# Kernel tuning notes

Measured on AMD Instinct MI355X. Metric: run time of the kernel, lower is better.

Reference implementation:

```python
import jax, jax.numpy as jnp
import numpy as np

ACT_DIM = 768
DICT_SIZE = 16384
K = 64
BATCH = 2048


def setup_inputs() -> dict:
    key = jax.random.key(0)
    k_x, k_w, k_be = jax.random.split(key, 3)
    x = jax.random.normal(k_x, (BATCH, ACT_DIM), dtype=jnp.float32)
    # encoder weight [dict_size, act_dim]; decoder initialized as encoder.T with unit-norm columns
    W_enc = jax.random.normal(k_w, (DICT_SIZE, ACT_DIM), dtype=jnp.float32) * 0.02
    b_enc = jnp.zeros((DICT_SIZE,), dtype=jnp.float32)
    W_dec = W_enc.T  # [act_dim, dict_size]
    eps = jnp.finfo(jnp.float32).eps
    W_dec = W_dec / (jnp.linalg.norm(W_dec, axis=0, keepdims=True) + eps)
    b_dec = jnp.zeros((ACT_DIM,), dtype=jnp.float32)
    return {"x": x, "W_enc": W_enc, "b_enc": b_enc, "W_dec": W_dec, "b_dec": b_dec}


def reference(x, W_enc, b_enc, W_dec, b_dec):
    B = x.shape[0]
    # encode: linear on (x - b_dec), relu
    post_relu_BF = jax.nn.relu((x - b_dec) @ W_enc.T + b_enc)  # [B, F]
    flat = post_relu_BF.reshape(-1)  # [B*F]
    # global batch top-k: keep k*B largest activations across the whole batch
    vals, idx = jax.lax.top_k(flat, K * B)
    encoded_flat = jnp.zeros_like(flat).at[idx].set(vals)
    encoded_BF = encoded_flat.reshape(post_relu_BF.shape)
    # decode
    x_hat_BD = encoded_BF @ W_dec.T + b_dec  # [B, D]
    return x_hat_BD
```

## Files before the change

### kernel.cpp

```cpp
#include <hip/hip_runtime.h>
#include <stdint.h>

#define BATCH   2048
#define DIM     768
#define FEAT    16384
#define KSEL    64
#define KB_SEL  (BATCH * KSEL)
#define N_TOT   (BATCH * FEAT)
#define NX4     (BATCH * DIM / 4)
#define NW4     (FEAT * DIM / 4)

#define GBM 128
#define GBN 128
#define GBK 32
#define AROW   24
#define APLANE 3088

#define SAMP_N  3072
#define CCAP    262144
#define TIE_CAP 1024
#define LSTAGE  2048
#define FG      8
#define FBLK    (CCAP / (FG * 4))

#define SL_T32    0
#define SL_NC     1
#define SL_DEF    2
#define SL_NTIE   3
#define SL_WIN    4
#define SL_S0     16

typedef __attribute__((ext_vector_type(8))) __bf16 bf16x8;
typedef __attribute__((ext_vector_type(4))) float  f32x4;
typedef unsigned long long u64;

__device__ __forceinline__ unsigned short bf16r(float v)
{
    unsigned u = __float_as_uint(v);
    u += 0x7FFFu + ((u >> 16) & 1u);
    return (unsigned short)(u >> 16);
}

__device__ __forceinline__ unsigned wave_append(unsigned* counter, bool pred)
{
    unsigned long long m = __ballot(pred);
    if (m == 0ull) return 0xFFFFFFFFu;
    const int lane = threadIdx.x & 63;
    const int leader = __ffsll((unsigned long long)m) - 1;
    unsigned base = 0;
    if (lane == leader) base = atomicAdd(counter, (unsigned)__popcll(m));
    base = __shfl(base, leader, 64);
    if (!pred) return 0xFFFFFFFFu;
    return base + (unsigned)__popcll(m & ((1ull << lane) - 1ull));
}

__global__ __launch_bounds__(256) void sae17_prep(const float* __restrict__ x,
                                                  const float* __restrict__ Wenc,
                                                  const float* __restrict__ bdec,
                                                  unsigned short* __restrict__ xb,
                                                  unsigned short* __restrict__ wb)
{
    const int tot = NX4 + NW4;
    for (int i = blockIdx.x * 256 + threadIdx.x; i < tot; i += gridDim.x * 256) {
        if (i < NX4) {
            const int e = i * 4;
            const int d = e % DIM;
            float4 v  = *(const float4*)(x + e);
            float4 dv = *(const float4*)(bdec + d);
            uint2 p;
            p.x = (unsigned)bf16r(v.x - dv.x) | ((unsigned)bf16r(v.y - dv.y) << 16);
            p.y = (unsigned)bf16r(v.z - dv.z) | ((unsigned)bf16r(v.w - dv.w) << 16);
            *(uint2*)(xb + e) = p;
        } else {
            const int e = (i - NX4) * 4;
            float4 v = *(const float4*)(Wenc + e);
            uint2 p;
            p.x = (unsigned)bf16r(v.x) | ((unsigned)bf16r(v.y) << 16);
            p.y = (unsigned)bf16r(v.z) | ((unsigned)bf16r(v.w) << 16);
            *(uint2*)(wb + e) = p;
        }
    }
}

__global__ __launch_bounds__(256) void sae17_gemm(const unsigned short* __restrict__ xb,
                                                  const unsigned short* __restrict__ wb,
                                                  const float* __restrict__ benc,
                                                  unsigned short* __restrict__ Yb)
{
    __shared__ unsigned short Als[4 * APLANE];
    __shared__ unsigned short Bls[4 * APLANE];

    const int tid  = threadIdx.x;
    const int row0 = blockIdx.y * GBM;
    const int col0 = blockIdx.x * GBN;
    const int wid  = tid >> 6;
    const int lane = tid & 63;
    const int wr = wid >> 1;
    const int wc = wid & 1;
    const int fr = lane & 15;
    const int kg = lane >> 4;

    f32x4 acc[4][4];
#pragma unroll
    for (int i = 0; i < 4; ++i)
#pragma unroll
        for (int j = 0; j < 4; ++j) acc[i][j] = (f32x4){0.f, 0.f, 0.f, 0.f};

    for (int kt = 0; kt < DIM; kt += GBK) {
#pragma unroll
        for (int i = 0; i < 4; ++i) {
            const int idx = i * 256 + tid;
            const int r   = idx >> 3;
            const int kq  = (idx & 7) * 4;
            const int g   = kq >> 3;
            const int k0  = kq & 7;
            *(uint2*)&Als[g * APLANE + r * AROW + k0] =
                *(const uint2*)(xb + (size_t)(row0 + r) * DIM + kt + kq);
            *(uint2*)&Bls[g * APLANE + r * AROW + k0] =
                *(const uint2*)(wb + (size_t)(col0 + r) * DIM + kt + kq);
        }
        __syncthreads();

        bf16x8 afr[4], bfr[4];
#pragma unroll
        for (int mi = 0; mi < 4; ++mi)
            afr[mi] = *(const bf16x8*)&Als[kg * APLANE + (wr * 64 + mi * 16 + fr) * AROW];
#pragma unroll
        for (int ni = 0; ni < 4; ++ni)
            bfr[ni] = *(const bf16x8*)&Bls[kg * APLANE + (wc * 64 + ni * 16 + fr) * AROW];
#pragma unroll
        for (int mi = 0; mi < 4; ++mi)
#pragma unroll
            for (int ni = 0; ni < 4; ++ni)
                acc[mi][ni] = __builtin_amdgcn_mfma_f32_16x16x32_bf16(
                    afr[mi], bfr[ni], acc[mi][ni], 0, 0, 0);
        __syncthreads();
    }

#pragma unroll
    for (int ni = 0; ni < 4; ++ni) {
        const int col = col0 + wc * 64 + ni * 16 + fr;
        const float be = benc[col];
#pragma unroll
        for (int mi = 0; mi < 4; ++mi) {
            const int rbase = row0 + wr * 64 + mi * 16 + kg * 4;
#pragma unroll
            for (int j = 0; j < 4; ++j)
                Yb[(size_t)(rbase + j) * FEAT + col] =
                    bf16r(fmaxf(acc[mi][ni][j] + be, 0.f));
        }
    }
}

__global__ void sae17_wt(const float* __restrict__ Wdec,
                         unsigned short* __restrict__ Wtb)
{
    __shared__ float t[32][33];
    const int f0 = blockIdx.x * 32;
    const int d0 = blockIdx.y * 32;
    const int tx = threadIdx.x;
    const int ty = threadIdx.y;
#pragma unroll
    for (int i = 0; i < 4; ++i)
        t[ty + i * 8][tx] = Wdec[(size_t)(d0 + ty + i * 8) * FEAT + f0 + tx];
    __syncthreads();
#pragma unroll
    for (int i = 0; i < 4; ++i)
        Wtb[(size_t)(f0 + ty + i * 8) * DIM + d0 + tx] = bf16r(t[tx][ty + i * 8]);
}

__global__ __launch_bounds__(256) void sae17_shist(const unsigned short* __restrict__ Yb,
                                                   unsigned* __restrict__ hist)
{
    __shared__ unsigned h[8192];
    const int t = threadIdx.x;
    for (int i = t; i < 8192; i += 256) h[i] = 0u;
    __syncthreads();
    const uint4* Y8 = (const uint4*)Yb;
    const int idx = blockIdx.x * 256 + t;
    const int i = idx * 64;
    if (i < N_TOT / 8) {
        uint4 v = Y8[i];
        unsigned w[4] = {v.x, v.y, v.z, v.w};
#pragma unroll
        for (int k = 0; k < 4; ++k) {
            unsigned lo = w[k] & 0xFFFFu;
            unsigned hi = w[k] >> 16;
            if (lo) atomicAdd(&h[lo >> 2], 1u);
            if (hi) atomicAdd(&h[hi >> 2], 1u);
        }
    }
    __syncthreads();
    for (int i2 = t; i2 < 8192; i2 += 256) {
        unsigned c = h[i2];
        if (c) atomicAdd(&hist[i2], c);
    }
}

__global__ __launch_bounds__(1024) void sae17_selb(const unsigned* __restrict__ hist,
                                                   unsigned* sl)
{
    __shared__ unsigned s[1024];
    const int t = threadIdx.x;
    const int C = 8;
    const unsigned N = (unsigned)SAMP_N;
    const int lo = t * C;
    unsigned S = 0;
    for (int i = 0; i < C; ++i) S += hist[lo + i];
    s[t] = S;
    __syncthreads();
    for (int off = 1; off < 1024; off <<= 1) {
        unsigned v = (t + off < 1024) ? s[t + off] : 0u;
        __syncthreads();
        s[t] += v;
        __syncthreads();
    }
    const unsigned incl  = s[t];
    const unsigned above = incl - S;
    if (above < N && N <= incl) {
        unsigned cum = above;
        for (int i = lo + C - 1; i >= lo; --i) {
            cum += hist[i];
            if (cum >= N) { sl[SL_T32] = (unsigned)i << 2; break; }
        }
    }
}

__global__ __launch_bounds__(256) void sae17_cand(const unsigned short* __restrict__ Yb,
                                                  unsigned* __restrict__ sl,
                                                  int* __restrict__ cand_raw)
{
    __shared__ int      loc[LSTAGE];
    __shared__ unsigned lcnt;
    __shared__ unsigned gbase;
    if (threadIdx.x == 0) lcnt = 0;
    __syncthreads();

    const unsigned T = sl[SL_T32];
    const uint4* Y8 = (const uint4*)Yb;
    const int total8 = N_TOT / 8;
    for (int i = blockIdx.x * blockDim.x + threadIdx.x; i < total8;
         i += gridDim.x * blockDim.x) {
        uint4 v = Y8[i];
        unsigned w[4] = {v.x, v.y, v.z, v.w};
#pragma unroll
        for (int k = 0; k < 4; ++k) {
            unsigned lo = w[k] & 0xFFFFu;
            unsigned hi = w[k] >> 16;
            if (lo >= T) {
                unsigned p = atomicAdd(&lcnt, 1u);
                if (p < (unsigned)LSTAGE) loc[p] = i * 8 + k * 2;
            }
            if (hi >= T) {
                unsigned p = atomicAdd(&lcnt, 1u);
                if (p < (unsigned)LSTAGE) loc[p] = i * 8 + k * 2 + 1;
            }
        }
    }
    __syncthreads();
    unsigned n = lcnt;
    if (n > (unsigned)LSTAGE) n = (unsigned)LSTAGE;
    if (threadIdx.x == 0) gbase = atomicAdd(&sl[SL_NC], n);
    __syncthreads();
    const unsigned base = gbase;
    for (unsigned k = threadIdx.x; k < n; k += blockDim.x) {
        unsigned dst = base + k;
        if (dst < (unsigned)CCAP) cand_raw[dst] = loc[k];
    }
}

__global__ __launch_bounds__(256) void sae17_fhist(const int* __restrict__ cand_raw,
                                                   const unsigned* __restrict__ sl,
                                                   unsigned* __restrict__ fhist)
{
    __shared__ unsigned h[16384];
    const int t = threadIdx.x;
    for (int i = t; i < 16384; i += 256) h[i] = 0u;
    __syncthreads();
    unsigned NC = sl[SL_NC];
    if (NC > (unsigned)CCAP) NC = (unsigned)CCAP;
    for (int i = blockIdx.x * 256 + t; i < (int)NC; i += gridDim.x * 256)
        atomicAdd(&h[cand_raw[i] & (FEAT - 1)], 1u);
    __syncthreads();
    for (int i = t; i < 16384; i += 256) {
        unsigned c = h[i];
        if (c) atomicAdd(&fhist[i], c);
    }
}

__global__ __launch_bounds__(1024) void sae17_fscan(const unsigned* __restrict__ fhist,
                                                    unsigned* __restrict__ fofs)
{
    __shared__ unsigned s[1024];
    const int t = threadIdx.x;
    unsigned c[16];
    unsigned sum = 0;
#pragma unroll
    for (int j = 0; j < 16; ++j) { c[j] = fhist[t * 16 + j]; sum += c[j]; }
    s[t] = sum;
    __syncthreads();
    for (int off = 1; off < 1024; off <<= 1) {
        unsigned v = (t >= off) ? s[t - off] : 0u;
        __syncthreads();
        s[t] += v;
        __syncthreads();
    }
    unsigned run = s[t] - sum;
#pragma unroll
    for (int j = 0; j < 16; ++j) { fofs[t * 16 + j] = run; run += c[j]; }
}

__global__ __launch_bounds__(256) void sae17_fscat(const int* __restrict__ cand_raw,
                                                   const unsigned* __restrict__ sl,
                                                   const unsigned* __restrict__ fofs,
                                                   unsigned* __restrict__ fcur,
                                                   int* __restrict__ cand_flat)
{
    unsigned NC = sl[SL_NC];
    if (NC > (unsigned)CCAP) NC = (unsigned)CCAP;
    for (int i = blockIdx.x * 256 + threadIdx.x; i < (int)NC; i += gridDim.x * 256) {
        int flat = cand_raw[i];
        int f = flat & (FEAT - 1);
        unsigned p = atomicAdd(&fcur[f], 1u);
        unsigned dst = fofs[f] + p;
        if (dst < (unsigned)CCAP) cand_flat[dst] = flat;
    }
}

__global__ __launch_bounds__(256) void sae17_feval(const float* __restrict__ x,
                                                   const float* __restrict__ Wenc,
                                                   const float* __restrict__ benc,
                                                   const float* __restrict__ bdec,
                                                   const unsigned* __restrict__ sl,
                                                   const int* __restrict__ cand_flat,
                                                   u64* __restrict__ cand_key)
{
    unsigned NC = sl[SL_NC];
    if (NC > (unsigned)CCAP) NC = (unsigned)CCAP;
    const int lane = threadIdx.x & 63;
    const int b = blockIdx.x;
    const int lb = (b & 7) * (FBLK / 8) + (b >> 3);
    const int wid = lb * 4 + (threadIdx.x >> 6);
    const int c0 = wid * FG;
    if (c0 >= (int)NC) return;

    float bd[12], wv[12];
#pragma unroll
    for (int j = 0; j < 12; ++j) bd[j] = bdec[lane + j * 64];
    int fprev = -1;

    for (int g = 0; g < FG; ++g) {
        const int c = c0 + g;
        if (c >= (int)NC) break;
        const int flat = cand_flat[c];
        const int bb = flat >> 14;
        const int f  = flat & (FEAT - 1);
        if (f != fprev) {
            const float* wr = Wenc + (size_t)f * DIM;
#pragma unroll
            for (int j = 0; j < 12; ++j) wv[j] = wr[lane + j * 64];
            fprev = f;
        }
        const float* xr = x + (size_t)bb * DIM;
        double p = 0.0;
#pragma unroll
        for (int j = 0; j < 12; ++j)
            p = fma((double)xr[lane + j * 64] - (double)bd[j], (double)wv[j], p);
#pragma unroll
        for (int o = 32; o > 0; o >>= 1) p += __shfl_xor(p, o, 64);
        if (lane == 0) {
            p += (double)benc[f];
            if (p < 0.0) p = 0.0;
            cand_key[c] = (u64)__double_as_longlong(p);
        }
    }
}

__global__ __launch_bounds__(256) void sae17_hist64(const u64* __restrict__ cand_key,
                                                    const unsigned* __restrict__ sl,
                                                    unsigned* __restrict__ hist,
                                                    int pass)
{
    __shared__ unsigned h[16384];
    const int t = threadIdx.x;
    for (int i = t; i < 16384; i += 256) h[i] = 0u;
    __syncthreads();

    unsigned NC = sl[SL_NC];
    if (NC > (unsigned)CCAP) NC = (unsigned)CCAP;
    u64 pref = 0;
    for (int i = 0; i < pass; ++i) pref = (pref << 14) | (u64)sl[SL_S0 + i];
    const int chk_sh = 64 - 14 * pass;
    const int bkt_sh = 50 - 14 * pass;

    for (int i = blockIdx.x * 256 + t; i < (int)NC; i += gridDim.x * 256) {
        u64 key = cand_key[i];
        if (pass > 0 && (key >> chk_sh) != pref) continue;
        atomicAdd(&h[(unsigned)(key >> bkt_sh) & 0x3FFFu], 1u);
    }
    __syncthreads();
    for (int i = t; i < 16384; i += 256) {
        unsigned c = h[i];
        if (c) atomicAdd(&hist[i], c);
    }
}

__global__ __launch_bounds__(1024) void sae17_sel14(const unsigned* __restrict__ hist,
                                                    unsigned* sl, int pass)
{
    __shared__ unsigned s[1024];
    const int t = threadIdx.x;
    const int C = 16;
    const unsigned N = (pass == 0) ? (unsigned)KB_SEL : sl[SL_S0 + 4 + pass - 1];
    const int lo = t * C;
    unsigned S = 0;
    for (int i = 0; i < C; ++i) S += hist[lo + i];
    s[t] = S;
    __syncthreads();
    for (int off = 1; off < 1024; off <<= 1) {
        unsigned v = (t + off < 1024) ? s[t + off] : 0u;
        __syncthreads();
        s[t] += v;
        __syncthreads();
    }
    const unsigned incl  = s[t];
    const unsigned above = incl - S;
    if (above < N && N <= incl) {
        unsigned cum = above;
        for (int i = lo + C - 1; i >= lo; --i) {
            cum += hist[i];
            if (cum >= N) {
                sl[SL_S0 + pass]     = (unsigned)i;
                sl[SL_S0 + 4 + pass] = N - (cum - hist[i]);
                break;
            }
        }
    }
}

__global__ __launch_bounds__(256) void sae17_maxb(const u64* __restrict__ cand_key,
                                                  const unsigned* __restrict__ sl,
                                                  u64* __restrict__ mx)
{
    unsigned NC = sl[SL_NC];
    if (NC > (unsigned)CCAP) NC = (unsigned)CCAP;
    const u64 Tsh1 = ((u64)sl[SL_S0 + 0] << 28) | ((u64)sl[SL_S0 + 1] << 14) |
                     (u64)sl[SL_S0 + 2];
    u64 m = 0;
    for (int i = blockIdx.x * 256 + threadIdx.x; i < (int)NC; i += gridDim.x * 256) {
        u64 k = cand_key[i];
        if ((k >> 22) < Tsh1 && k > m) m = k;
    }
#pragma unroll
    for (int o = 32; o > 0; o >>= 1) {
        u64 o2 = __shfl_xor(m, o, 64);
        if (o2 > m) m = o2;
    }
    if ((threadIdx.x & 63) == 0 && m) atomicMax((unsigned long long*)mx, m);
}

__global__ __launch_bounds__(256) void sae17_class(const u64* __restrict__ cand_key,
                                                   const int* __restrict__ cand_flat,
                                                   const u64* __restrict__ mx,
                                                   unsigned* __restrict__ sl,
                                                   unsigned* __restrict__ row_cnt,
                                                   int* __restrict__ sel_flat,
                                                   float* __restrict__ sel_val,
                                                   int* __restrict__ tie_flat,
                                                   u64* __restrict__ tie_key)
{
    unsigned NC = sl[SL_NC];
    if (NC > (unsigned)CCAP) NC = (unsigned)CCAP;
    const u64 Tsh1 = ((u64)sl[SL_S0 + 0] << 28) | ((u64)sl[SL_S0 + 1] << 14) |
                     (u64)sl[SL_S0 + 2];
    const u64 Tsh2 = mx[0] >> 22;
    const int c = blockIdx.x * 256 + threadIdx.x;
    const bool active = (c < (int)NC);
    u64 key = 0;
    int flat = 0;
    u64 keysh = 0;
    if (active) {
        key = cand_key[c];
        keysh = key >> 22;
        flat = cand_flat[c];
    }
    const bool selp = active && (keysh > Tsh1);
    unsigned p = wave_append(&sl[SL_DEF], selp);
    if (selp && p < (unsigned)KB_SEL) {
        sel_flat[p] = flat;
        sel_val[p]  = (float)__longlong_as_double((long long)key);
        atomicAdd(&row_cnt[flat >> 14], 1u);
    }
    const bool tiep = active && !selp && (keysh == Tsh2);
    unsigned q = wave_append(&sl[SL_NTIE], tiep);
    if (tiep && q < (unsigned)TIE_CAP) { tie_flat[q] = flat; tie_key[q] = key; }
}

__global__ __launch_bounds__(256) void sae17_ties(const int* __restrict__ tie_flat,
                                                  const u64* __restrict__ tie_key,
                                                  unsigned* __restrict__ sl,
                                                  int* __restrict__ sel_flat,
                                                  float* __restrict__ sel_val,
                                                  unsigned* __restrict__ row_cnt)
{
    unsigned R = sl[SL_NTIE];
    if (R > (unsigned)TIE_CAP) R = (unsigned)TIE_CAP;
    const unsigned REM = sl[SL_S0 + 6];
    const unsigned D = sl[SL_DEF];
    const int c = blockIdx.x * blockDim.x + threadIdx.x;
    if (c >= (int)R) return;
    const int ic = tie_flat[c];
    unsigned rank = 0;
    for (int j = 0; j < (int)R; ++j)
        if (tie_flat[j] < ic) ++rank;
    if (rank < REM) {
        unsigned p = D + atomicAdd(&sl[SL_WIN], 1u);
        if (p < (unsigned)KB_SEL) {
            sel_flat[p] = ic;
            sel_val[p]  = (float)__longlong_as_double((long long)tie_key[c]);
            atomicAdd(&row_cnt[ic >> 14], 1u);
        }
    }
}

__global__ __launch_bounds__(256) void sae17_scan(const unsigned* __restrict__ row_cnt,
                                                  unsigned* __restrict__ row_ofs)
{
    __shared__ unsigned s[256];
    const int t = threadIdx.x;
    unsigned c[8];
    unsigned sum = 0;
#pragma unroll
    for (int j = 0; j < 8; ++j) { c[j] = row_cnt[t * 8 + j]; sum += c[j]; }
    s[t] = sum;
    __syncthreads();
    for (int off = 1; off < 256; off <<= 1) {
        unsigned v = (t >= off) ? s[t - off] : 0u;
        __syncthreads();
        s[t] += v;
        __syncthreads();
    }
    unsigned run = s[t] - sum;
#pragma unroll
    for (int j = 0; j < 8; ++j) { row_ofs[t * 8 + j] = run; run += c[j]; }
    if (t == 255) row_ofs[2048] = run;
}

__global__ void sae17_scatter(const int* __restrict__ sel_flat,
                              const float* __restrict__ sel_val,
                              const unsigned* __restrict__ row_ofs,
                              unsigned* __restrict__ cursor,
                              int* __restrict__ gf, float* __restrict__ gv)
{
    int e = blockIdx.x * blockDim.x + threadIdx.x;
    if (e >= KB_SEL) return;
    int flat = sel_flat[e];
    int b = flat >> 14;
    unsigned p = atomicAdd(&cursor[b], 1u);
    unsigned dst = row_ofs[b] + p;
    if (dst < (unsigned)KB_SEL) {
        gf[dst] = flat & (FEAT - 1);
        gv[dst] = sel_val[e];
    }
}

__global__ __launch_bounds__(256) void sae17_decode(const int* __restrict__ gf,
                                                    const float* __restrict__ gv,
                                                    const unsigned* __restrict__ row_ofs,
                                                    const unsigned short* __restrict__ Wtb,
                                                    const float* __restrict__ bdec,
                                                    float* __restrict__ out)
{
    const int b = blockIdx.x;
    const int t = threadIdx.x;
    float a0 = 0.f, a1 = 0.f, a2 = 0.f;
    const unsigned s = row_ofs[b];
    const unsigned e = row_ofs[b + 1];
    for (unsigned i = s; i < e; ++i) {
        const int f   = gf[i];
        const float v = gv[i];
        const unsigned short* w = Wtb + (size_t)f * DIM;
        a0 = fmaf(v, __uint_as_float((unsigned)w[t]       << 16), a0);
        a1 = fmaf(v, __uint_as_float((unsigned)w[t + 256] << 16), a1);
        a2 = fmaf(v, __uint_as_float((unsigned)w[t + 512] << 16), a2);
    }
    out[(size_t)b * DIM + t]       = a0 + bdec[t];
    out[(size_t)b * DIM + t + 256] = a1 + bdec[t + 256];
    out[(size_t)b * DIM + t + 512] = a2 + bdec[t + 512];
}

extern "C" void kernel_launch(void* const* d_in, const int* in_sizes, int n_in,
                              void* d_out, int out_size, void* d_ws, size_t ws_size,
                              hipStream_t stream)
{
    (void)in_sizes; (void)n_in; (void)out_size;
    const float* x    = (const float*)d_in[0];
    const float* Wenc = (const float*)d_in[1];
    const float* benc = (const float*)d_in[2];
    const float* Wdec = (const float*)d_in[3];
    const float* bdec = (const float*)d_in[4];
    float* out = (float*)d_out;

    char* ws = (char*)d_ws;
    size_t off = 0;
    unsigned short* Yb  = (unsigned short*)(ws + off);     off += (size_t)N_TOT * 2;
    unsigned short* Wtb = (unsigned short*)(ws + off);     off += (size_t)FEAT * DIM * 2;
    unsigned short* xb  = (unsigned short*)(ws + off);     off += (size_t)BATCH * DIM * 2;
    unsigned short* wb  = (unsigned short*)(ws + off);     off += (size_t)FEAT * DIM * 2;
    u64*      cand_key  = (u64*)(ws + off);                off += (size_t)CCAP * 8;
    int*      cand_raw  = (int*)(ws + off);                off += (size_t)CCAP * 4;
    int*      cand_flat = (int*)(ws + off);                off += (size_t)CCAP * 4;
    int*      tie_flat  = (int*)(ws + off);                off += (size_t)TIE_CAP * 4;
    u64*      tie_key   = (u64*)(ws + off);                off += (size_t)TIE_CAP * 8;
    unsigned* row_ofs   = (unsigned*)(ws + off);           off += 2052 * 4;
    unsigned* fofs      = (unsigned*)(ws + off);           off += 16384 * 4;
    char* zstart = ws + off;
    int*      sel_flat  = (int*)(ws + off);                off += (size_t)KB_SEL * 4;
    float*    sel_val   = (float*)(ws + off);              off += (size_t)KB_SEL * 4;
    int*      gf        = (int*)(ws + off);                off += (size_t)KB_SEL * 4;
    float*    gv        = (float*)(ws + off);              off += (size_t)KB_SEL * 4;
    unsigned* hist1     = (unsigned*)(ws + off);           off += 8192 * 4;
    unsigned* h64       = (unsigned*)(ws + off);           off += 3 * 16384 * 4;
    unsigned* fhist     = (unsigned*)(ws + off);           off += 16384 * 4;
    unsigned* fcur      = (unsigned*)(ws + off);           off += 16384 * 4;
    unsigned* row_cnt   = (unsigned*)(ws + off);           off += 2048 * 4;
    unsigned* cursor    = (unsigned*)(ws + off);           off += 2048 * 4;
    u64*      mx        = (u64*)(ws + off);                off += 8;
    unsigned* sl        = (unsigned*)(ws + off);           off += 256;
    const size_t zbytes = (size_t)((ws + off) - zstart);
    if (ws_size < off) return;

    hipMemsetAsync(zstart, 0, zbytes, stream);

    sae17_prep<<<4096, 256, 0, stream>>>(x, Wenc, bdec, xb, wb);
    sae17_wt<<<dim3(FEAT / 32, DIM / 32), dim3(32, 8), 0, stream>>>(Wdec, Wtb);
    sae17_gemm<<<dim3(FEAT / GBN, BATCH / GBM), 256, 0, stream>>>(xb, wb, benc, Yb);

    sae17_shist<<<256, 256, 0, stream>>>(Yb, hist1);
    sae17_selb<<<1, 1024, 0, stream>>>(hist1, sl);

    sae17_cand<<<2048, 256, 0, stream>>>(Yb, sl, cand_raw);
    sae17_fhist<<<256, 256, 0, stream>>>(cand_raw, sl, fhist);
    sae17_fscan<<<1, 1024, 0, stream>>>(fhist, fofs);
    sae17_fscat<<<256, 256, 0, stream>>>(cand_raw, sl, fofs, fcur, cand_flat);
    sae17_feval<<<FBLK, 256, 0, stream>>>(x, Wenc, benc, bdec, sl, cand_flat, cand_key);

    for (int p = 0; p < 3; ++p) {
        sae17_hist64<<<256, 256, 0, stream>>>(cand_key, sl, h64 + p * 16384, p);
        sae17_sel14<<<1, 1024, 0, stream>>>(h64 + p * 16384, sl, p);
    }
    sae17_maxb<<<256, 256, 0, stream>>>(cand_key, sl, mx);

    sae17_class<<<(CCAP + 255) / 256, 256, 0, stream>>>(cand_key, cand_flat, mx, sl, row_cnt,
                                                        sel_flat, sel_val, tie_flat, tie_key);
    sae17_ties<<<TIE_CAP / 256, 256, 0, stream>>>(tie_flat, tie_key, sl,
                                                  sel_flat, sel_val, row_cnt);

    sae17_scan<<<1, 256, 0, stream>>>(row_cnt, row_ofs);
    sae17_scatter<<<(KB_SEL + 255) / 256, 256, 0, stream>>>(sel_flat, sel_val, row_ofs, cursor, gf, gv);
    sae17_decode<<<BATCH, 256, 0, stream>>>(gf, gv, row_ofs, Wtb, bdec, out);
}
```

Measured before the change: 449.1 us.

## Fuse candidate thresholding into encoder GEMM and sample histogram from first row block

The full bf16 pre-activation matrix is no longer written to global memory. A first GEMM pass computes only the first 128 batch rows and builds the threshold histogram directly from its accumulators. A second full GEMM then applies the threshold in its epilogue and appends candidate indices, replacing the separate histogram and candidate scan kernels. This removes a large write and re-read of the activation matrix at the cost of extra GEMM work for the sample rows. It also makes the threshold estimate depend on the first rows being representative of the whole batch.

Result: faster. 434.7 us (-3.2%).

```diff
diff --git a/kernel.cpp b/kernel.cpp
--- a/kernel.cpp
+++ b/kernel.cpp
@@ -16,12 +16,13 @@
 #define AROW   24
 #define APLANE 3088
 
-#define SAMP_N  3072
-#define CCAP    262144
-#define TIE_CAP 1024
-#define LSTAGE  2048
-#define FG      8
-#define FBLK    (CCAP / (FG * 4))
+#define SAMP_ROWS 128
+#define SAMP_N    12288
+#define CCAP      262144
+#define TIE_CAP   1024
+#define LSTAGE    2048
+#define FG        8
+#define FBLK      (CCAP / (FG * 4))
 
 #define SL_T32    0
 #define SL_NC     1
@@ -54,7 +55,7 @@
     return base + (unsigned)__popcll(m & ((1ull << lane) - 1ull));
 }
 
-__global__ __launch_bounds__(256) void sae17_prep(const float* __restrict__ x,
+__global__ __launch_bounds__(256) void sae18_prep(const float* __restrict__ x,
                                                   const float* __restrict__ Wenc,
                                                   const float* __restrict__ bdec,
                                                   unsigned short* __restrict__ xb,
@@ -82,16 +83,18 @@
     }
 }
 
-__global__ __launch_bounds__(256) void sae17_gemm(const unsigned short* __restrict__ xb,
-                                                  const unsigned short* __restrict__ wb,
-                                                  const float* __restrict__ benc,
-                                                  unsigned short* __restrict__ Yb)
+__global__ __launch_bounds__(256) void sae18_sgemm(const unsigned short* __restrict__ xb,
+                                                   const unsigned short* __restrict__ wb,
+                                                   const float* __restrict__ benc,
+                                                   unsigned* __restrict__ hist)
 {
     __shared__ unsigned short Als[4 * APLANE];
     __shared__ unsigned short Bls[4 * APLANE];
+    __shared__ unsigned h[8192];
 
     const int tid  = threadIdx.x;
-    const int row0 = blockIdx.y * GBM;
+    for (int i = tid; i < 8192; i += 256) h[i] = 0u;
+    const int row0 = 0;
     const int col0 = blockIdx.x * GBN;
     const int wid  = tid >> 6;
     const int lane = tid & 63;
@@ -143,61 +146,21 @@
         const float be = benc[col];
 #pragma unroll
         for (int mi = 0; mi < 4; ++mi) {
-            const int rbase = row0 + wr * 64 + mi * 16 + kg * 4;
-#pragma unroll
-            for (int j = 0; j < 4; ++j)
-                Yb[(size_t)(rbase + j) * FEAT + col] =
-                    bf16r(fmaxf(acc[mi][ni][j] + be, 0.f));
-        }
-    }
-}
-
-__global__ void sae17_wt(const float* __restrict__ Wdec,
-                         unsigned short* __restrict__ Wtb)
-{
-    __shared__ float t[32][33];
-    const int f0 = blockIdx.x * 32;
-    const int d0 = blockIdx.y * 32;
-    const int tx = threadIdx.x;
-    const int ty = threadIdx.y;
-#pragma unroll
-    for (int i = 0; i < 4; ++i)
-        t[ty + i * 8][tx] = Wdec[(size_t)(d0 + ty + i * 8) * FEAT + f0 + tx];
-    __syncthreads();
-#pragma unroll
-    for (int i = 0; i < 4; ++i)
-        Wtb[(size_t)(f0 + ty + i * 8) * DIM + d0 + tx] = bf16r(t[tx][ty + i * 8]);
-}
-
-__global__ __launch_bounds__(256) void sae17_shist(const unsigned short* __restrict__ Yb,
-                                                   unsigned* __restrict__ hist)
-{
-    __shared__ unsigned h[8192];
-    const int t = threadIdx.x;
-    for (int i = t; i < 8192; i += 256) h[i] = 0u;
-    __syncthreads();
-    const uint4* Y8 = (const uint4*)Yb;
-    const int idx = blockIdx.x * 256 + t;
-    const int i = idx * 64;
-    if (i < N_TOT / 8) {
-        uint4 v = Y8[i];
-        unsigned w[4] = {v.x, v.y, v.z, v.w};
-#pragma unroll
-        for (int k = 0; k < 4; ++k) {
-            unsigned lo = w[k] & 0xFFFFu;
-            unsigned hi = w[k] >> 16;
-            if (lo) atomicAdd(&h[lo >> 2], 1u);
-            if (hi) atomicAdd(&h[hi >> 2], 1u);
-        }
-    }
-    __syncthreads();
-    for (int i2 = t; i2 < 8192; i2 += 256) {
-        unsigned c = h[i2];
-        if (c) atomicAdd(&hist[i2], c);
-    }
-}
-
-__global__ __launch_bounds__(1024) void sae17_selb(const unsigned* __restrict__ hist,
+#pragma unroll
+            for (int j = 0; j < 4; ++j) {
+                unsigned short bits = bf16r(fmaxf(acc[mi][ni][j] + be, 0.f));
+                if (bits) atomicAdd(&h[bits >> 2], 1u);
+            }
+        }
+    }
+    __syncthreads();
+    for (int i = tid; i < 8192; i += 256) {
+        unsigned c = h[i];
+        if (c) atomicAdd(&hist[i], c);
+    }
+}
+
+__global__ __launch_bounds__(1024) void sae18_selb(const unsigned* __restrict__ hist,
                                                    unsigned* sl)
 {
     __shared__ unsigned s[1024];
@@ -226,50 +189,114 @@
     }
 }
 
-__global__ __launch_bounds__(256) void sae17_cand(const unsigned short* __restrict__ Yb,
+__global__ __launch_bounds__(256) void sae18_gemm(const unsigned short* __restrict__ xb,
+                                                  const unsigned short* __restrict__ wb,
+                                                  const float* __restrict__ benc,
                                                   unsigned* __restrict__ sl,
                                                   int* __restrict__ cand_raw)
 {
+    __shared__ unsigned short Als[4 * APLANE];
+    __shared__ unsigned short Bls[4 * APLANE];
     __shared__ int      loc[LSTAGE];
     __shared__ unsigned lcnt;
     __shared__ unsigned gbase;
-    if (threadIdx.x == 0) lcnt = 0;
-    __syncthreads();
+
+    const int tid  = threadIdx.x;
+    if (tid == 0) lcnt = 0;
+    const int row0 = blockIdx.y * GBM;
+    const int col0 = blockIdx.x * GBN;
+    const int wid  = tid >> 6;
+    const int lane = tid & 63;
+    const int wr = wid >> 1;
+    const int wc = wid & 1;
+    const int fr = lane & 15;
+    const int kg = lane >> 4;
+
+    f32x4 acc[4][4];
+#pragma unroll
+    for (int i = 0; i < 4; ++i)
+#pragma unroll
+        for (int j = 0; j < 4; ++j) acc[i][j] = (f32x4){0.f, 0.f, 0.f, 0.f};
+
+    for (int kt = 0; kt < DIM; kt += GBK) {
+#pragma unroll
+        for (int i = 0; i < 4; ++i) {
+            const int idx = i * 256 + tid;
+            const int r   = idx >> 3;
+            const int kq  = (idx & 7) * 4;
+            const int g   = kq >> 3;
+            const int k0  = kq & 7;
+            *(uint2*)&Als[g * APLANE + r * AROW + k0] =
+                *(const uint2*)(xb + (size_t)(row0 + r) * DIM + kt + kq);
+            *(uint2*)&Bls[g * APLANE + r * AROW + k0] =
+                *(const uint2*)(wb + (size_t)(col0 + r) * DIM + kt + kq);
+        }
+        __syncthreads();
+
+        bf16x8 afr[4], bfr[4];
+#pragma unroll
+        for (int mi = 0; mi < 4; ++mi)
+            afr[mi] = *(const bf16x8*)&Als[kg * APLANE + (wr * 64 + mi * 16 + fr) * AROW];
+#pragma unroll
+        for (int ni = 0; ni < 4; ++ni)
+            bfr[ni] = *(const bf16x8*)&Bls[kg * APLANE + (wc * 64 + ni * 16 + fr) * AROW];
+#pragma unroll
+        for (int mi = 0; mi < 4; ++mi)
+#pragma unroll
+            for (int ni = 0; ni < 4; ++ni)
+                acc[mi][ni] = __builtin_amdgcn_mfma_f32_16x16x32_bf16(
+                    afr[mi], bfr[ni], acc[mi][ni], 0, 0, 0);
+        __syncthreads();
+    }
 
     const unsigned T = sl[SL_T32];
-    const uint4* Y8 = (const uint4*)Yb;
-    const int total8 = N_TOT / 8;
-    for (int i = blockIdx.x * blockDim.x + threadIdx.x; i < total8;
-         i += gridDim.x * blockDim.x) {
-        uint4 v = Y8[i];
-        unsigned w[4] = {v.x, v.y, v.z, v.w};
-#pragma unroll
-        for (int k = 0; k < 4; ++k) {
-            unsigned lo = w[k] & 0xFFFFu;
-            unsigned hi = w[k] >> 16;
-            if (lo >= T) {
-                unsigned p = atomicAdd(&lcnt, 1u);
-                if (p < (unsigned)LSTAGE) loc[p] = i * 8 + k * 2;
-            }
-            if (hi >= T) {
-                unsigned p = atomicAdd(&lcnt, 1u);
-                if (p < (unsigned)LSTAGE) loc[p] = i * 8 + k * 2 + 1;
+#pragma unroll
+    for (int ni = 0; ni < 4; ++ni) {
+        const int col = col0 + wc * 64 + ni * 16 + fr;
+        const float be = benc[col];
+#pragma unroll
+        for (int mi = 0; mi < 4; ++mi) {
+            const int rbase = row0 + wr * 64 + mi * 16 + kg * 4;
+#pragma unroll
+            for (int j = 0; j < 4; ++j) {
+                unsigned short bits = bf16r(fmaxf(acc[mi][ni][j] + be, 0.f));
+                if ((unsigned)bits >= T) {
+                    unsigned p = atomicAdd(&lcnt, 1u);
+                    if (p < (unsigned)LSTAGE) loc[p] = (rbase + j) * FEAT + col;
+                }
             }
         }
     }
     __syncthreads();
     unsigned n = lcnt;
     if (n > (unsigned)LSTAGE) n = (unsigned)LSTAGE;
-    if (threadIdx.x == 0) gbase = atomicAdd(&sl[SL_NC], n);
+    if (tid == 0) gbase = atomicAdd(&sl[SL_NC], n);
     __syncthreads();
     const unsigned base = gbase;
-    for (unsigned k = threadIdx.x; k < n; k += blockDim.x) {
+    for (unsigned k = tid; k < n; k += 256) {
         unsigned dst = base + k;
         if (dst < (unsigned)CCAP) cand_raw[dst] = loc[k];
     }
 }
 
-__global__ __launch_bounds__(256) void sae17_fhist(const int* __restrict__ cand_raw,
+__global__ void sae18_wt(const float* __restrict__ Wdec,
+                         unsigned short* __restrict__ Wtb)
+{
+    __shared__ float t[32][33];
+    const int f0 = blockIdx.x * 32;
+    const int d0 = blockIdx.y * 32;
+    const int tx = threadIdx.x;
+    const int ty = threadIdx.y;
+#pragma unroll
+    for (int i = 0; i < 4; ++i)
+        t[ty + i * 8][tx] = Wdec[(size_t)(d0 + ty + i * 8) * FEAT + f0 + tx];
+    __syncthreads();
+#pragma unroll
+    for (int i = 0; i < 4; ++i)
+        Wtb[(size_t)(f0 + ty + i * 8) * DIM + d0 + tx] = bf16r(t[tx][ty + i * 8]);
+}
+
+__global__ __launch_bounds__(256) void sae18_fhist(const int* __restrict__ cand_raw,
                                                    const unsigned* __restrict__ sl,
                                                    unsigned* __restrict__ fhist)
 {
@@ -288,7 +315,7 @@
     }
 }
 
-__global__ __launch_bounds__(1024) void sae17_fscan(const unsigned* __restrict__ fhist,
+__global__ __launch_bounds__(1024) void sae18_fscan(const unsigned* __restrict__ fhist,
                                                     unsigned* __restrict__ fofs)
 {
     __shared__ unsigned s[1024];
@@ -310,7 +337,7 @@
     for (int j = 0; j < 16; ++j) { fofs[t * 16 + j] = run; run += c[j]; }
 }
 
-__global__ __launch_bounds__(256) void sae17_fscat(const int* __restrict__ cand_raw,
+__global__ __launch_bounds__(256) void sae18_fscat(const int* __restrict__ cand_raw,
                                                    const unsigned* __restrict__ sl,
                                                    const unsigned* __restrict__ fofs,
                                                    unsigned* __restrict__ fcur,
@@ -327,7 +354,7 @@
     }
 }
 
-__global__ __launch_bounds__(256) void sae17_feval(const float* __restrict__ x,
+__global__ __launch_bounds__(256) void sae18_feval(const float* __restrict__ x,
                                                    const float* __restrict__ Wenc,
                                                    const float* __restrict__ benc,
                                                    const float* __restrict__ bdec,
@@ -376,7 +403,7 @@
     }
 }
 
-__global__ __launch_bounds__(256) void sae17_hist64(const u64* __restrict__ cand_key,
+__global__ __launch_bounds__(256) void sae18_hist64(const u64* __restrict__ cand_key,
                                                     const unsigned* __restrict__ sl,
                                                     unsigned* __restrict__ hist,
                                                     int pass)
@@ -405,7 +432,7 @@
     }
 }
 
-__global__ __launch_bounds__(1024) void sae17_sel14(const unsigned* __restrict__ hist,
+__global__ __launch_bounds__(1024) void sae18_sel14(const unsigned* __restrict__ hist,
                                                     unsigned* sl, int pass)
 {
     __shared__ unsigned s[1024];
@@ -438,7 +465,7 @@
     }
 }
 
-__global__ __launch_bounds__(256) void sae17_maxb(const u64* __restrict__ cand_key,
+__global__ __launch_bounds__(256) void sae18_maxb(const u64* __restrict__ cand_key,
                                                   const unsigned* __restrict__ sl,
                                                   u64* __restrict__ mx)
 {
@@ -459,7 +486,7 @@
     if ((threadIdx.x & 63) == 0 && m) atomicMax((unsigned long long*)mx, m);
 }
 
-__global__ __launch_bounds__(256) void sae17_class(const u64* __restrict__ cand_key,
+__global__ __launch_bounds__(256) void sae18_class(const u64* __restrict__ cand_key,
                                                    const int* __restrict__ cand_flat,
                                                    const u64* __restrict__ mx,
                                                    unsigned* __restrict__ sl,
@@ -496,7 +523,7 @@
     if (tiep && q < (unsigned)TIE_CAP) { tie_flat[q] = flat; tie_key[q] = key; }
 }
 
-__global__ __launch_bounds__(256) void sae17_ties(const int* __restrict__ tie_flat,
+__global__ __launch_bounds__(256) void sae18_ties(const int* __restrict__ tie_flat,
                                                   const u64* __restrict__ tie_key,
                                                   unsigned* __restrict__ sl,
                                                   int* __restrict__ sel_flat,
@@ -523,7 +550,7 @@
     }
 }
 
-__global__ __launch_bounds__(256) void sae17_scan(const unsigned* __restrict__ row_cnt,
+__global__ __launch_bounds__(256) void sae18_scan(const unsigned* __restrict__ row_cnt,
                                                   unsigned* __restrict__ row_ofs)
 {
     __shared__ unsigned s[256];
@@ -546,7 +573,7 @@
     if (t == 255) row_ofs[2048] = run;
 }
 
-__global__ void sae17_scatter(const int* __restrict__ sel_flat,
+__global__ void sae18_scatter(const int* __restrict__ sel_flat,
                               const float* __restrict__ sel_val,
                               const unsigned* __restrict__ row_ofs,
                               unsigned* __restrict__ cursor,
@@ -564,7 +591,7 @@
     }
 }
 
-__global__ __launch_bounds__(256) void sae17_decode(const int* __restrict__ gf,
+__global__ __launch_bounds__(256) void sae18_decode(const int* __restrict__ gf,
                                                     const float* __restrict__ gv,
                                                     const unsigned* __restrict__ row_ofs,
                                                     const unsigned short* __restrict__ Wtb,
@@ -603,7 +630,6 @@
 
     char* ws = (char*)d_ws;
     size_t off = 0;
-    unsigned short* Yb  = (unsigned short*)(ws + off);     off += (size_t)N_TOT * 2;
     unsigned short* Wtb = (unsigned short*)(ws + off);     off += (size_t)FEAT * DIM * 2;
     unsigned short* xb  = (unsigned short*)(ws + off);     off += (size_t)BATCH * DIM * 2;
     unsigned short* wb  = (unsigned short*)(ws + off);     off += (size_t)FEAT * DIM * 2;
@@ -632,31 +658,31 @@
 
     hipMemsetAsync(zstart, 0, zbytes, stream);
 
-    sae17_prep<<<4096, 256, 0, stream>>>(x, Wenc, bdec, xb, wb);
-    sae17_wt<<<dim3(FEAT / 32, DIM / 32), dim3(32, 8), 0, stream>>>(Wdec, Wtb);
-    sae17_gemm<<<dim3(FEAT / GBN, BATCH / GBM), 256, 0, stream>>>(xb, wb, benc, Yb);
-
-    sae17_shist<<<256, 256, 0, stream>>>(Yb, hist1);
-    sae17_selb<<<1, 1024, 0, stream>>>(hist1, sl);
-
-    sae17_cand<<<2048, 256, 0, stream>>>(Yb, sl, cand_raw);
-    sae17_fhist<<<256, 256, 0, stream>>>(cand_raw, sl, fhist);
-    sae17_fscan<<<1, 1024, 0, stream>>>(fhist, fofs);
-    sae17_fscat<<<256, 256, 0, stream>>>(cand_raw, sl, fofs, fcur, cand_flat);
-    sae17_feval<<<FBLK, 256, 0, stream>>>(x, Wenc, benc, bdec, sl, cand_flat, cand_key);
+    sae18_prep<<<4096, 256, 0, stream>>>(x, Wenc, bdec, xb, wb);
+    sae18_wt<<<dim3(FEAT / 32, DIM / 32), dim3(32, 8), 0, stream>>>(Wdec, Wtb);
+
+    sae18_sgemm<<<dim3(FEAT / GBN, 1), 256, 0, stream>>>(xb, wb, benc, hist1);
+    sae18_selb<<<1, 1024, 0, stream>>>(hist1, sl);
+
+    sae18_gemm<<<dim3(FEAT / GBN, BATCH / GBM), 256, 0, stream>>>(xb, wb, benc, sl, cand_raw);
+
+    sae18_fhist<<<256, 256, 0, stream>>>(cand_raw, sl, fhist);
+    sae18_fscan<<<1, 1024, 0, stream>>>(fhist, fofs);
+    sae18_fscat<<<256, 256, 0, stream>>>(cand_raw, sl, fofs, fcur, cand_flat);
+    sae18_feval<<<FBLK, 256, 0, stream>>>(x, Wenc, benc, bdec, sl, cand_flat, cand_key);
 
     for (int p = 0; p < 3; ++p) {
-        sae17_hist64<<<256, 256, 0, stream>>>(cand_key, sl, h64 + p * 16384, p);
-        sae17_sel14<<<1, 1024, 0, stream>>>(h64 + p * 16384, sl, p);
-    }
-    sae17_maxb<<<256, 256, 0, stream>>>(cand_key, sl, mx);
-
-    sae17_class<<<(CCAP + 255) / 256, 256, 0, stream>>>(cand_key, cand_flat, mx, sl, row_cnt,
+        sae18_hist64<<<256, 256, 0, stream>>>(cand_key, sl, h64 + p * 16384, p);
+        sae18_sel14<<<1, 1024, 0, stream>>>(h64 + p * 16384, sl, p);
+    }
+    sae18_maxb<<<256, 256, 0, stream>>>(cand_key, sl, mx);
+
+    sae18_class<<<(CCAP + 255) / 256, 256, 0, stream>>>(cand_key, cand_flat, mx, sl, row_cnt,
                                                         sel_flat, sel_val, tie_flat, tie_key);
-    sae17_ties<<<TIE_CAP / 256, 256, 0, stream>>>(tie_flat, tie_key, sl,
+    sae18_ties<<<TIE_CAP / 256, 256, 0, stream>>>(tie_flat, tie_key, sl,
                                                   sel_flat, sel_val, row_cnt);
 
-    sae17_scan<<<1, 256, 0, stream>>>(row_cnt, row_ofs);
-    sae17_scatter<<<(KB_SEL + 255) / 256, 256, 0, stream>>>(sel_flat, sel_val, row_ofs, cursor, gf, gv);
-    sae17_decode<<<BATCH, 256, 0, stream>>>(gf, gv, row_ofs, Wtb, bdec, out);
-}
+    sae18_scan<<<1, 256, 0, stream>>>(row_cnt, row_ofs);
+    sae18_scatter<<<(KB_SEL + 255) / 256, 256, 0, stream>>>(sel_flat, sel_val, row_ofs, cursor, gf, gv);
+    sae18_decode<<<BATCH, 256, 0, stream>>>(gf, gv, row_ofs, Wtb, bdec, out);
+}
```
